# Optimization experiments

Measured on AMD Instinct MI355X. Metric: run time of the kernel, lower is better.

Reference implementation:

```python
import jax, jax.numpy as jnp
import numpy as np

B, C, H, W = 4, 256, 64, 64
CI = C // 2  # inter_channels


def setup_inputs() -> dict:
    key = jax.random.key(0)
    ks = jax.random.split(key, 10)
    s_in = 1.0 / np.sqrt(C)
    s_out = 1.0 / np.sqrt(CI)
    return {
        "rgbd": jax.random.normal(ks[0], (B, C, H, W), jnp.float32),
        "x": jax.random.normal(ks[1], (B, C, H, W), jnp.float32),
        "q_w": jax.random.uniform(ks[2], (CI, C), jnp.float32, -s_in, s_in),
        "q_b": jax.random.uniform(ks[3], (CI,), jnp.float32, -s_in, s_in),
        "k_w": jax.random.uniform(ks[4], (CI, C), jnp.float32, -s_in, s_in),
        "k_b": jax.random.uniform(ks[5], (CI,), jnp.float32, -s_in, s_in),
        "v_w": jax.random.uniform(ks[6], (CI, C), jnp.float32, -s_in, s_in),
        "v_b": jax.random.uniform(ks[7], (CI,), jnp.float32, -s_in, s_in),
        "out_w": jax.random.uniform(ks[8], (C, CI), jnp.float32, -s_out, s_out),
        "out_b": jax.random.uniform(ks[9], (C,), jnp.float32, -s_out, s_out),
    }


def reference(rgbd, x, q_w, q_b, k_w, k_b, v_w, v_b, out_w, out_b):
    b, c, h, w = rgbd.shape
    ci = q_w.shape[0]
    n = h * w
    # 1x1 convs == channel-wise linear maps; flatten spatial to tokens
    xs = x.reshape(b, c, n)        # [B, C, N]
    rs = rgbd.reshape(b, c, n)     # [B, C, N]
    q = jnp.einsum('oc,bcn->bno', q_w, xs) + q_b          # [B, N, CI]
    k = jnp.einsum('oc,bcn->bon', k_w, rs) + k_b[:, None]  # [B, CI, N]
    v = jnp.einsum('oc,bcn->bno', v_w, rs) + v_b          # [B, N, CI]
    attn = jax.nn.softmax(jnp.einsum('bqc,bck->bqk', q, k), axis=-1)  # [B, N, N]
    out = jnp.einsum('bqk,bkc->bqc', attn, v)             # [B, N, CI]
    out = jnp.einsum('oc,bnc->bon', out_w, out) + out_b[:, None]  # [B, C, N]
    return rgbd + out.reshape(b, c, h, w)
```

## Files before the change

### kernel.cpp

```cpp
#include <hip/hip_runtime.h>
#include <cstdint>
#include <cstddef>

typedef unsigned short u16;
typedef __attribute__((ext_vector_type(8))) short bf16x8;
typedef __attribute__((ext_vector_type(4))) float f32x4;
typedef __attribute__((ext_vector_type(16))) float f32x16;
typedef __attribute__((ext_vector_type(4))) uint32_t u32x4;

#define DEV __device__ __forceinline__

static constexpr float LOG2E = 1.4426950408889634f;

DEV u16 f2bf(float f) {
  uint32_t u = __float_as_uint(f);
  u += 0x7fffu + ((u >> 16) & 1u);
  return (u16)(u >> 16);
}
DEV float bf2f(u16 h) {
  uint32_t u = ((uint32_t)h) << 16;
  return __uint_as_float(u);
}
DEV uint32_t cvtpk(float lo, float hi) {
  uint32_t r;
  asm("v_cvt_pk_bf16_f32 %0, %1, %2" : "=v"(r) : "v"(lo), "v"(hi));
  return r;
}
DEV float exp2fast(float x) {
  float r;
  asm("v_exp_f32 %0, %1" : "=v"(r) : "v"(x));
  return r;
}
DEV void plswap(uint32_t& a, uint32_t& b) {
  asm("v_permlane32_swap_b32 %0, %1" : "+v"(a), "+v"(b));
}

DEV f32x4 mfma16(bf16x8 a, bf16x8 b, f32x4 c) {
  return __builtin_amdgcn_mfma_f32_16x16x32_bf16(a, b, c, 0, 0, 0);
}
DEV f32x16 mfma32(bf16x8 a, bf16x8 b, f32x16 c) {
  return __builtin_amdgcn_mfma_f32_32x32x16_bf16(a, b, c, 0, 0, 0);
}

DEV void gload_lds16(const void* g, void* l) {
  __builtin_amdgcn_global_load_lds(
      (const __attribute__((address_space(1))) uint32_t*)g,
      (__attribute__((address_space(3))) uint32_t*)l, 16, 0, 0);
}

static constexpr int BATCH = 4;
static constexpr int C = 256;
static constexpr int CI = 128;
static constexpr int N = 4096;
static constexpr int SPLIT = 4;

__global__ __launch_bounds__(256) void cvt_w(const float* __restrict__ a,
                                             const float* __restrict__ b,
                                             const float* __restrict__ c,
                                             const float* __restrict__ d,
                                             u16* __restrict__ oa, u16* __restrict__ ob,
                                             u16* __restrict__ oc, u16* __restrict__ od) {
  int i = blockIdx.x * 256 + threadIdx.x;
  oa[i] = f2bf(a[i] * LOG2E);
  ob[i] = f2bf(b[i]);
  oc[i] = f2bf(c[i]);
  od[i] = f2bf(d[i]);
}

__global__ __launch_bounds__(256) void proj_kernel(
    const float* __restrict__ x, const float* __restrict__ rgbd,
    const u16* __restrict__ Wq, const u16* __restrict__ Wk, const u16* __restrict__ Wv,
    const float* __restrict__ qb, const float* __restrict__ kb, const float* __restrict__ vb,
    u16* __restrict__ Qb, u16* __restrict__ Kb, u16* __restrict__ Vtb) {
  __shared__ __align__(16) u16 xT[64][C + 8];
  __shared__ __align__(16) u16 rT[64][C + 8];
  const int b = blockIdx.y;
  const int n0 = blockIdx.x * 64;
  const int t = threadIdx.x;
  {
    const int tok = t & 63, cp = (t >> 6) * 2;
    const float* xb = x + (size_t)b * C * N + n0;
    const float* rb = rgbd + (size_t)b * C * N + n0;
    for (int c0 = 0; c0 < C; c0 += 8) {
      int c = c0 + cp;
      *(uint32_t*)&xT[tok][c] = cvtpk(xb[(size_t)c * N + tok], xb[(size_t)(c + 1) * N + tok]);
      *(uint32_t*)&rT[tok][c] = cvtpk(rb[(size_t)c * N + tok], rb[(size_t)(c + 1) * N + tok]);
    }
  }
  __syncthreads();
  const int w = t >> 6, lane = t & 63, g = lane >> 4, cl = lane & 15;

#define PROJ_QK(Sarr, W, bias, Out, SCL)                                              \
  {                                                                                   \
    bf16x8 afr[8];                                                                    \
    _Pragma("unroll") for (int ks = 0; ks < 8; ++ks)                                  \
        afr[ks] = *(const bf16x8*)&Sarr[w * 16 + cl][ks * 32 + g * 8];                \
    _Pragma("unroll") for (int ct = 0; ct < 8; ++ct) {                                \
      f32x4 acc = {0.f, 0.f, 0.f, 0.f};                                               \
      _Pragma("unroll") for (int ks = 0; ks < 8; ++ks) {                              \
        bf16x8 bb = *(const bf16x8*)&W[(size_t)(ct * 16 + cl) * C + ks * 32 + g * 8]; \
        acc = mfma16(afr[ks], bb, acc);                                               \
      }                                                                               \
      float bv = bias[ct * 16 + cl] * (SCL);                                          \
      _Pragma("unroll") for (int r = 0; r < 4; ++r) {                                 \
        int tok = n0 + w * 16 + g * 4 + r;                                            \
        Out[((size_t)b * N + tok) * CI + ct * 16 + cl] = f2bf(acc[r] + bv);           \
      }                                                                               \
    }                                                                                 \
  }

  PROJ_QK(xT, Wq, qb, Qb, LOG2E)
  PROJ_QK(rT, Wk, kb, Kb, 1.0f)
#undef PROJ_QK

  #pragma unroll
  for (int rt = 0; rt < 2; ++rt) {
    bf16x8 aw[8];
    #pragma unroll
    for (int ks = 0; ks < 8; ++ks)
      aw[ks] = *(const bf16x8*)&Wv[(size_t)(w * 32 + rt * 16 + cl) * C + ks * 32 + g * 8];
    #pragma unroll
    for (int ct = 0; ct < 4; ++ct) {
      f32x4 acc = {0.f, 0.f, 0.f, 0.f};
      #pragma unroll
      for (int ks = 0; ks < 8; ++ks) {
        bf16x8 bb = *(const bf16x8*)&rT[ct * 16 + cl][ks * 32 + g * 8];
        acc = mfma16(aw[ks], bb, acc);
      }
      #pragma unroll
      for (int r = 0; r < 4; ++r) {
        int o = w * 32 + rt * 16 + g * 4 + r;
        Vtb[((size_t)b * CI + o) * N + n0 + ct * 16 + cl] = f2bf(acc[r] + vb[o]);
      }
    }
  }
}

template <int SPL>
__global__ __launch_bounds__(128, 2) void attn_kernel(
    const u16* __restrict__ Qb, const u16* __restrict__ Kb,
    const u16* __restrict__ Vtb, u16* __restrict__ Opart,
    float2* __restrict__ ml) {
  constexpr int KPB = N / SPL;
  constexpr int NT = KPB / 32;
  constexpr int CPX = 32 * SPL;
  __shared__ __align__(16) u16 Klds[2][32 * 128];
  __shared__ __align__(16) u16 Vlds[2][128 * 32];
  const int lin = blockIdx.x;
  const int nl = (lin & 7) * CPX + (lin >> 3);
  const int qi = nl & 63;
  const int grp = nl >> 6;
  const int b = grp & 3;
  const int s = grp >> 2;
  const int q0 = qi * 64;
  const int t = threadIdx.x;
  const int w = t >> 6, lane = t & 63;
  const int hi = lane >> 5, l31 = lane & 31;

  const u16* Kg = Kb + (size_t)b * N * CI;
  const u16* Vg = Vtb + (size_t)b * CI * N;

  const int v_ss = (t & 3) ^ ((t >> 3) & 3);
  const int wbase = (t & ~63);

#define STAGE_KV(bi, k0_)                                                         \
  do {                                                                            \
    _Pragma("unroll") for (int c = 0; c < 4; ++c) {                               \
      const int r = c * 8 + (t >> 4);                                             \
      const int ss = (t & 15) ^ (r & 15);                                         \
      gload_lds16(Kg + (size_t)((k0_) + r) * CI + ss * 8,                         \
                  &Klds[bi][(c * 128 + wbase) * 8]);                              \
    }                                                                             \
    _Pragma("unroll") for (int c = 0; c < 4; ++c) {                               \
      const int vr = c * 32 + (t >> 2);                                           \
      gload_lds16(Vg + (size_t)vr * N + (k0_) + v_ss * 8,                         \
                  &Vlds[bi][(c * 128 + wbase) * 8]);                              \
    }                                                                             \
  } while (0)

  const u16* Qg = Qb + ((size_t)b * N + q0 + w * 32 + l31) * CI;
  bf16x8 qf[8];
  #pragma unroll
  for (int mm = 0; mm < 8; ++mm)
    qf[mm] = *(const bf16x8*)(Qg + mm * 16 + hi * 8);
  asm volatile("s_waitcnt vmcnt(0)" ::: "memory");

  f32x16 oacc[4];
  #pragma unroll
  for (int ct = 0; ct < 4; ++ct)
    #pragma unroll
    for (int i = 0; i < 16; ++i) oacc[ct][i] = 0.f;
  float m_run = -1e30f, l_run = 0.f;

  const int kbeg = s * KPB;
  STAGE_KV(0, kbeg);
  STAGE_KV(1, kbeg + 32);

  int buf = 0;
  for (int tt = 0; tt < NT; ++tt) {
    asm volatile("s_waitcnt vmcnt(8)" ::: "memory");
    __builtin_amdgcn_s_barrier();
    const int knext = kbeg + ((tt + 2 < NT) ? tt + 2 : tt) * 32;

    bf16x8 kf[8];
    #pragma unroll
    for (int mm = 0; mm < 8; ++mm)
      kf[mm] = *(const bf16x8*)&Klds[buf][l31 * 128 + ((((mm << 1) | hi) ^ l31) & 15) * 8];
    bf16x8 vf[4][2];
    const int vsw = (l31 >> 1) & 3;
    #pragma unroll
    for (int ct = 0; ct < 4; ++ct)
      #pragma unroll
      for (int ks = 0; ks < 2; ++ks)
        vf[ct][ks] = *(const bf16x8*)
            &Vlds[buf][(32 * ct + l31) * 32 + ((((ks << 1) | hi) ^ vsw) & 3) * 8];
    asm volatile("s_waitcnt lgkmcnt(0)" ::: "memory");
    __builtin_amdgcn_sched_barrier(0);
    __builtin_amdgcn_s_barrier();
    STAGE_KV(buf, knext);

    f32x16 st;
    #pragma unroll
    for (int i = 0; i < 16; ++i) st[i] = 0.f;
    __builtin_amdgcn_s_setprio(1);
    #pragma unroll
    for (int mm = 0; mm < 8; ++mm) st = mfma32(kf[mm], qf[mm], st);
    __builtin_amdgcn_s_setprio(0);

    float tmax = st[0];
    #pragma unroll
    for (int i = 1; i < 16; ++i) tmax = fmaxf(tmax, st[i]);
    tmax = fmaxf(tmax, __shfl_xor(tmax, 32));
    if (!__all(tmax - m_run <= 11.5f)) {
      const float mn = fmaxf(m_run, tmax);
      const float alpha = exp2fast(m_run - mn);
      m_run = mn;
      l_run *= alpha;
      #pragma unroll
      for (int reg = 0; reg < 16; ++reg) {
        float ar = __shfl(alpha, (reg & 3) + 8 * (reg >> 2) + 4 * hi);
        oacc[0][reg] *= ar; oacc[1][reg] *= ar;
        oacc[2][reg] *= ar; oacc[3][reg] *= ar;
      }
    }
    float p[16];
    float ls = 0.f;
    #pragma unroll
    for (int i = 0; i < 16; ++i) {
      p[i] = exp2fast(st[i] - m_run);
      ls += p[i];
    }
    ls += __shfl_xor(ls, 32);
    l_run += ls;

    uint32_t d0 = cvtpk(p[0], p[1]),   e0 = cvtpk(p[4], p[5]);
    uint32_t d1 = cvtpk(p[2], p[3]),   e1 = cvtpk(p[6], p[7]);
    uint32_t d2 = cvtpk(p[8], p[9]),   e2 = cvtpk(p[12], p[13]);
    uint32_t d3 = cvtpk(p[10], p[11]), e3 = cvtpk(p[14], p[15]);
    plswap(d0, e0);
    plswap(d1, e1);
    plswap(d2, e2);
    plswap(d3, e3);
    u32x4 pw0 = {d0, d1, e0, e1};
    u32x4 pw1 = {d2, d3, e2, e3};
    bf16x8 pa0 = __builtin_bit_cast(bf16x8, pw0);
    bf16x8 pa1 = __builtin_bit_cast(bf16x8, pw1);

    __builtin_amdgcn_s_setprio(1);
    #pragma unroll
    for (int ct = 0; ct < 4; ++ct) {
      oacc[ct] = mfma32(pa0, vf[ct][0], oacc[ct]);
      oacc[ct] = mfma32(pa1, vf[ct][1], oacc[ct]);
    }
    __builtin_amdgcn_s_setprio(0);

    buf ^= 1;
  }
#undef STAGE_KV
  asm volatile("s_waitcnt vmcnt(0)" ::: "memory");

  const float inv = 1.0f / l_run;
  #pragma unroll
  for (int reg = 0; reg < 16; ++reg) {
    const int ql = (reg & 3) + 8 * (reg >> 2) + 4 * hi;
    const float invr = __shfl(inv, ql);
    const int q = q0 + w * 32 + ql;
    #pragma unroll
    for (int ct = 0; ct < 4; ++ct)
      Opart[(((size_t)(s * BATCH + b)) * N + q) * CI + 32 * ct + l31] =
          f2bf(oacc[ct][reg] * invr);
  }
  if (lane < 32) {
    const int q = q0 + w * 32 + lane;
    ml[(size_t)(s * BATCH + b) * N + q] = make_float2(m_run, l_run);
  }
}

__global__ __launch_bounds__(256) void outproj_kernel(
    const u16* __restrict__ Opart, const float2* __restrict__ ml,
    const u16* __restrict__ Wo, const float* __restrict__ obias,
    const float* __restrict__ rgbd, float* __restrict__ out) {
  __shared__ __align__(16) u16 ObL[64][CI + 8];
  const int b = blockIdx.y;
  const int n0 = blockIdx.x * 64;
  const int t = threadIdx.x;

  #pragma unroll
  for (int i = 0; i < 4; ++i) {
    const int idx = t + i * 256;
    const int row_l = idx >> 4, ci8 = idx & 15;
    const size_t row = (size_t)b * N + n0 + row_l;
    float2 sv[SPLIT];
    float M = -1e30f;
    #pragma unroll
    for (int sp = 0; sp < SPLIT; ++sp) {
      sv[sp] = ml[(size_t)sp * BATCH * N + row];
      M = fmaxf(M, sv[sp].x);
    }
    float wv[SPLIT], wsum = 0.f;
    #pragma unroll
    for (int sp = 0; sp < SPLIT; ++sp) {
      wv[sp] = sv[sp].y * exp2fast(sv[sp].x - M);
      wsum += wv[sp];
    }
    const float invL = 1.0f / wsum;
    float acc[8];
    #pragma unroll
    for (int j = 0; j < 8; ++j) acc[j] = 0.f;
    #pragma unroll
    for (int sp = 0; sp < SPLIT; ++sp) {
      const float wsc = wv[sp] * invL;
      bf16x8 v = *(const bf16x8*)&Opart[((size_t)sp * BATCH * N + row) * CI + ci8 * 8];
      #pragma unroll
      for (int j = 0; j < 8; ++j) acc[j] += wsc * bf2f((u16)v[j]);
    }
    bf16x8 o;
    #pragma unroll
    for (int j = 0; j < 8; ++j) o[j] = (short)f2bf(acc[j]);
    *(bf16x8*)&ObL[row_l][ci8 * 8] = o;
  }
  __syncthreads();

  const int w = t >> 6, lane = t & 63, g = lane >> 4, cl = lane & 15;
  f32x4 acc[4][4];
  #pragma unroll
  for (int i = 0; i < 4; ++i)
    #pragma unroll
    for (int j = 0; j < 4; ++j) acc[i][j] = {0.f, 0.f, 0.f, 0.f};

  #pragma unroll
  for (int ks = 0; ks < 4; ++ks) {
    bf16x8 bo[4];
    #pragma unroll
    for (int ct = 0; ct < 4; ++ct)
      bo[ct] = *(const bf16x8*)&ObL[ct * 16 + cl][ks * 32 + g * 8];
    #pragma unroll
    for (int rt = 0; rt < 4; ++rt) {
      bf16x8 aw = *(const bf16x8*)&Wo[(size_t)(w * 64 + rt * 16 + cl) * CI + ks * 32 + g * 8];
      #pragma unroll
      for (int ct = 0; ct < 4; ++ct) acc[rt][ct] = mfma16(aw, bo[ct], acc[rt][ct]);
    }
  }
  #pragma unroll
  for (int rt = 0; rt < 4; ++rt) {
    #pragma unroll
    for (int r = 0; r < 4; ++r) {
      const int o = w * 64 + rt * 16 + g * 4 + r;
      const float bb = obias[o];
      #pragma unroll
      for (int ct = 0; ct < 4; ++ct) {
        size_t idx = ((size_t)b * C + o) * N + n0 + ct * 16 + cl;
        out[idx] = rgbd[idx] + bb + acc[rt][ct][r];
      }
    }
  }
}

extern "C" void kernel_launch(void* const* d_in, const int* in_sizes, int n_in,
                              void* d_out, int out_size, void* d_ws, size_t ws_size,
                              hipStream_t stream) {
  (void)in_sizes; (void)n_in; (void)out_size; (void)ws_size;
  const float* rgbd = (const float*)d_in[0];
  const float* x    = (const float*)d_in[1];
  const float* q_w  = (const float*)d_in[2];
  const float* q_b  = (const float*)d_in[3];
  const float* k_w  = (const float*)d_in[4];
  const float* k_b  = (const float*)d_in[5];
  const float* v_w  = (const float*)d_in[6];
  const float* v_b  = (const float*)d_in[7];
  const float* o_w  = (const float*)d_in[8];
  const float* o_b  = (const float*)d_in[9];
  float* out = (float*)d_out;

  char* ws = (char*)d_ws;
  const size_t MB = 1024 * 1024;
  const size_t szQKV = (size_t)BATCH * N * CI * sizeof(u16);
  u16* Qb  = (u16*)(ws);
  u16* Kb  = (u16*)(ws + szQKV);
  u16* Vtb = (u16*)(ws + 2 * szQKV);
  u16* Wq  = (u16*)(ws + 3 * szQKV);
  u16* Wk  = Wq + (size_t)CI * C;
  u16* Wv  = Wk + (size_t)CI * C;
  u16* Wo  = Wv + (size_t)CI * C;
  u16* Opart = (u16*)(ws + 13 * MB);
  float2* ml = (float2*)(ws + 29 * MB);

  cvt_w<<<dim3((C * CI) / 256), 256, 0, stream>>>(q_w, k_w, v_w, o_w, Wq, Wk, Wv, Wo);
  proj_kernel<<<dim3(N / 64, BATCH), 256, 0, stream>>>(x, rgbd, Wq, Wk, Wv,
                                                       q_b, k_b, v_b, Qb, Kb, Vtb);
  attn_kernel<SPLIT><<<dim3(64 * BATCH * SPLIT), 128, 0, stream>>>(Qb, Kb, Vtb, Opart, ml);
  outproj_kernel<<<dim3(N / 64, BATCH), 256, 0, stream>>>(Opart, ml, Wo, o_b, rgbd, out);
}
```

Measured before the change: 93.81 us.

## Double attention block and KV tile sizes, interleave two softmax halves

The attention kernel now uses 256-thread blocks covering 128 queries and stages 64-key K/V tiles, so each staged tile is shared by four waves instead of two. It halves the grid and the number of barrier iterations. Each iteration splits into two 32-key halves, with the PV MFMAs of the first half overlapping the QK MFMAs of the second. The projection kernel is retiled to 32 tokens per block with an occupancy hint, giving more blocks. The cost is doubled LDS per attention block and higher register pressure, which may limit occupancy.

```diff
diff --git a/kernel.cpp b/kernel.cpp
--- a/kernel.cpp
+++ b/kernel.cpp
@@ -67,21 +67,22 @@
   od[i] = f2bf(d[i]);
 }
 
-__global__ __launch_bounds__(256) void proj_kernel(
+__global__ __launch_bounds__(256, 4) void proj_kernel(
     const float* __restrict__ x, const float* __restrict__ rgbd,
     const u16* __restrict__ Wq, const u16* __restrict__ Wk, const u16* __restrict__ Wv,
     const float* __restrict__ qb, const float* __restrict__ kb, const float* __restrict__ vb,
     u16* __restrict__ Qb, u16* __restrict__ Kb, u16* __restrict__ Vtb) {
-  __shared__ __align__(16) u16 xT[64][C + 8];
-  __shared__ __align__(16) u16 rT[64][C + 8];
+  __shared__ __align__(16) u16 xT[32][C + 8];
+  __shared__ __align__(16) u16 rT[32][C + 8];
   const int b = blockIdx.y;
-  const int n0 = blockIdx.x * 64;
+  const int n0 = blockIdx.x * 32;
   const int t = threadIdx.x;
   {
-    const int tok = t & 63, cp = (t >> 6) * 2;
+    const int tok = t & 31, cp = (t >> 5) * 2;
     const float* xb = x + (size_t)b * C * N + n0;
     const float* rb = rgbd + (size_t)b * C * N + n0;
-    for (int c0 = 0; c0 < C; c0 += 8) {
+    #pragma unroll
+    for (int c0 = 0; c0 < C; c0 += 16) {
       int c = c0 + cp;
       *(uint32_t*)&xT[tok][c] = cvtpk(xb[(size_t)c * N + tok], xb[(size_t)(c + 1) * N + tok]);
       *(uint32_t*)&rT[tok][c] = cvtpk(rb[(size_t)c * N + tok], rb[(size_t)(c + 1) * N + tok]);
@@ -89,22 +90,25 @@
   }
   __syncthreads();
   const int w = t >> 6, lane = t & 63, g = lane >> 4, cl = lane & 15;
+  const int tg = w & 1;
+  const int hf = w >> 1;
 
 #define PROJ_QK(Sarr, W, bias, Out, SCL)                                              \
   {                                                                                   \
     bf16x8 afr[8];                                                                    \
     _Pragma("unroll") for (int ks = 0; ks < 8; ++ks)                                  \
-        afr[ks] = *(const bf16x8*)&Sarr[w * 16 + cl][ks * 32 + g * 8];                \
-    _Pragma("unroll") for (int ct = 0; ct < 8; ++ct) {                                \
+        afr[ks] = *(const bf16x8*)&Sarr[tg * 16 + cl][ks * 32 + g * 8];               \
+    _Pragma("unroll") for (int ct = 0; ct < 4; ++ct) {                                \
+      const int ctt = hf * 4 + ct;                                                    \
       f32x4 acc = {0.f, 0.f, 0.f, 0.f};                                               \
       _Pragma("unroll") for (int ks = 0; ks < 8; ++ks) {                              \
-        bf16x8 bb = *(const bf16x8*)&W[(size_t)(ct * 16 + cl) * C + ks * 32 + g * 8]; \
-        acc = mfma16(afr[ks], bb, acc);                                               \
+        bf16x8 bb = *(const bf16x8*)&W[(size_t)(ctt * 16 + cl) * C + ks * 32 + g * 8];\
+      acc = mfma16(afr[ks], bb, acc);                                                 \
       }                                                                               \
-      float bv = bias[ct * 16 + cl] * (SCL);                                          \
+      float bv = bias[ctt * 16 + cl] * (SCL);                                         \
       _Pragma("unroll") for (int r = 0; r < 4; ++r) {                                 \
-        int tok = n0 + w * 16 + g * 4 + r;                                            \
-        Out[((size_t)b * N + tok) * CI + ct * 16 + cl] = f2bf(acc[r] + bv);           \
+        int tok = n0 + tg * 16 + g * 4 + r;                                           \
+        Out[((size_t)b * N + tok) * CI + ctt * 16 + cl] = f2bf(acc[r] + bv);          \
       }                                                                               \
     }                                                                                 \
   }
@@ -120,7 +124,7 @@
     for (int ks = 0; ks < 8; ++ks)
       aw[ks] = *(const bf16x8*)&Wv[(size_t)(w * 32 + rt * 16 + cl) * C + ks * 32 + g * 8];
     #pragma unroll
-    for (int ct = 0; ct < 4; ++ct) {
+    for (int ct = 0; ct < 2; ++ct) {
       f32x4 acc = {0.f, 0.f, 0.f, 0.f};
       #pragma unroll
       for (int ks = 0; ks < 8; ++ks) {
@@ -137,22 +141,22 @@
 }
 
 template <int SPL>
-__global__ __launch_bounds__(128, 2) void attn_kernel(
+__global__ __launch_bounds__(256, 2) void attn_kernel(
     const u16* __restrict__ Qb, const u16* __restrict__ Kb,
     const u16* __restrict__ Vtb, u16* __restrict__ Opart,
     float2* __restrict__ ml) {
   constexpr int KPB = N / SPL;
-  constexpr int NT = KPB / 32;
-  constexpr int CPX = 32 * SPL;
-  __shared__ __align__(16) u16 Klds[2][32 * 128];
-  __shared__ __align__(16) u16 Vlds[2][128 * 32];
+  constexpr int NT = KPB / 64;
+  constexpr int CPX = 16 * SPL;
+  __shared__ __align__(16) u16 Klds[2][64 * 128];
+  __shared__ __align__(16) u16 Vlds[2][128 * 64];
   const int lin = blockIdx.x;
   const int nl = (lin & 7) * CPX + (lin >> 3);
-  const int qi = nl & 63;
-  const int grp = nl >> 6;
+  const int qi = nl & 31;
+  const int grp = nl >> 5;
   const int b = grp & 3;
   const int s = grp >> 2;
-  const int q0 = qi * 64;
+  const int q0 = qi * 128;
   const int t = threadIdx.x;
   const int w = t >> 6, lane = t & 63;
   const int hi = lane >> 5, l31 = lane & 31;
@@ -160,21 +164,20 @@
   const u16* Kg = Kb + (size_t)b * N * CI;
   const u16* Vg = Vtb + (size_t)b * CI * N;
 
-  const int v_ss = (t & 3) ^ ((t >> 3) & 3);
-  const int wbase = (t & ~63);
+  const int k_ss = (t & 15) ^ ((t >> 4) & 15);
+  const int v_ss = (t & 7) ^ ((t >> 3) & 7);
 
 #define STAGE_KV(bi, k0_)                                                         \
   do {                                                                            \
     _Pragma("unroll") for (int c = 0; c < 4; ++c) {                               \
-      const int r = c * 8 + (t >> 4);                                             \
-      const int ss = (t & 15) ^ (r & 15);                                         \
-      gload_lds16(Kg + (size_t)((k0_) + r) * CI + ss * 8,                         \
-                  &Klds[bi][(c * 128 + wbase) * 8]);                              \
+      const int r = c * 16 + (t >> 4);                                            \
+      gload_lds16(Kg + (size_t)((k0_) + r) * CI + k_ss * 8,                       \
+                  &Klds[bi][(c * 256 + t) * 8]);                                  \
     }                                                                             \
     _Pragma("unroll") for (int c = 0; c < 4; ++c) {                               \
-      const int vr = c * 32 + (t >> 2);                                           \
+      const int vr = c * 32 + (t >> 3);                                           \
       gload_lds16(Vg + (size_t)vr * N + (k0_) + v_ss * 8,                         \
-                  &Vlds[bi][(c * 128 + wbase) * 8]);                              \
+                  &Vlds[bi][(c * 256 + t) * 8]);                                  \
     }                                                                             \
   } while (0)
 
@@ -194,89 +197,120 @@
 
   const int kbeg = s * KPB;
   STAGE_KV(0, kbeg);
-  STAGE_KV(1, kbeg + 32);
+  STAGE_KV(1, kbeg + 64);
+
+#define SOFTMAX_HALF(st, paX0, paX1)                                              \
+  {                                                                               \
+    float tmax = st[0];                                                           \
+    _Pragma("unroll") for (int i = 1; i < 16; ++i) tmax = fmaxf(tmax, st[i]);     \
+    tmax = fmaxf(tmax, __shfl_xor(tmax, 32));                                     \
+    if (!__all(tmax - m_run <= 11.5f)) {                                          \
+      const float mn = fmaxf(m_run, tmax);                                        \
+      const float alpha = exp2fast(m_run - mn);                                   \
+      m_run = mn;                                                                 \
+      l_run *= alpha;                                                             \
+      _Pragma("unroll") for (int reg = 0; reg < 16; ++reg) {                      \
+        float ar = __shfl(alpha, (reg & 3) + 8 * (reg >> 2) + 4 * hi);            \
+        oacc[0][reg] *= ar; oacc[1][reg] *= ar;                                   \
+        oacc[2][reg] *= ar; oacc[3][reg] *= ar;                                   \
+      }                                                                           \
+    }                                                                             \
+    float p[16], ls = 0.f;                                                        \
+    _Pragma("unroll") for (int i = 0; i < 16; ++i) {                              \
+      p[i] = exp2fast(st[i] - m_run);                                             \
+      ls += p[i];                                                                 \
+    }                                                                             \
+    ls += __shfl_xor(ls, 32);                                                     \
+    l_run += ls;                                                                  \
+    uint32_t d0 = cvtpk(p[0], p[1]),   e0 = cvtpk(p[4], p[5]);                    \
+    uint32_t d1 = cvtpk(p[2], p[3]),   e1 = cvtpk(p[6], p[7]);                    \
+    uint32_t d2 = cvtpk(p[8], p[9]),   e2 = cvtpk(p[12], p[13]);                  \
+    uint32_t d3 = cvtpk(p[10], p[11]), e3 = cvtpk(p[14], p[15]);                  \
+    plswap(d0, e0); plswap(d1, e1); plswap(d2, e2); plswap(d3, e3);               \
+    u32x4 pw0 = {d0, d1, e0, e1};                                                 \
+    u32x4 pw1 = {d2, d3, e2, e3};                                                 \
+    paX0 = __builtin_bit_cast(bf16x8, pw0);                                       \
+    paX1 = __builtin_bit_cast(bf16x8, pw1);                                       \
+  }
 
   int buf = 0;
   for (int tt = 0; tt < NT; ++tt) {
     asm volatile("s_waitcnt vmcnt(8)" ::: "memory");
     __builtin_amdgcn_s_barrier();
-    const int knext = kbeg + ((tt + 2 < NT) ? tt + 2 : tt) * 32;
-
-    bf16x8 kf[8];
+    const int knext = kbeg + ((tt + 2 < NT) ? tt + 2 : tt) * 64;
+
+    bf16x8 kfA[8];
     #pragma unroll
     for (int mm = 0; mm < 8; ++mm)
-      kf[mm] = *(const bf16x8*)&Klds[buf][l31 * 128 + ((((mm << 1) | hi) ^ l31) & 15) * 8];
-    bf16x8 vf[4][2];
-    const int vsw = (l31 >> 1) & 3;
+      kfA[mm] = *(const bf16x8*)&Klds[buf][l31 * 128 + ((((mm << 1) | hi) ^ (l31 & 15)) & 15) * 8];
+    asm volatile("s_waitcnt lgkmcnt(0)" ::: "memory");
+    __builtin_amdgcn_sched_barrier(0);
+
+    f32x16 st0;
+    #pragma unroll
+    for (int i = 0; i < 16; ++i) st0[i] = 0.f;
+    __builtin_amdgcn_s_setprio(1);
+    #pragma unroll
+    for (int mm = 0; mm < 8; ++mm) st0 = mfma32(kfA[mm], qf[mm], st0);
+    __builtin_amdgcn_s_setprio(0);
+
+    bf16x8 paA0, paA1;
+    SOFTMAX_HALF(st0, paA0, paA1)
+
+    bf16x8 kfB[8];
+    #pragma unroll
+    for (int mm = 0; mm < 8; ++mm)
+      kfB[mm] = *(const bf16x8*)&Klds[buf][(32 + l31) * 128 + ((((mm << 1) | hi) ^ (l31 & 15)) & 15) * 8];
+    bf16x8 vfA[4][2];
     #pragma unroll
     for (int ct = 0; ct < 4; ++ct)
       #pragma unroll
       for (int ks = 0; ks < 2; ++ks)
-        vf[ct][ks] = *(const bf16x8*)
-            &Vlds[buf][(32 * ct + l31) * 32 + ((((ks << 1) | hi) ^ vsw) & 3) * 8];
+        vfA[ct][ks] = *(const bf16x8*)
+            &Vlds[buf][(32 * ct + l31) * 64 + ((((ks << 1) | hi) ^ (l31 & 7)) & 7) * 8];
+    asm volatile("s_waitcnt lgkmcnt(0)" ::: "memory");
+    __builtin_amdgcn_sched_barrier(0);
+
+    f32x16 st1;
+    #pragma unroll
+    for (int i = 0; i < 16; ++i) st1[i] = 0.f;
+    __builtin_amdgcn_s_setprio(1);
+    #pragma unroll
+    for (int ct = 0; ct < 4; ++ct) {
+      oacc[ct] = mfma32(paA0, vfA[ct][0], oacc[ct]);
+      oacc[ct] = mfma32(paA1, vfA[ct][1], oacc[ct]);
+    }
+    #pragma unroll
+    for (int mm = 0; mm < 8; ++mm) st1 = mfma32(kfB[mm], qf[mm], st1);
+    __builtin_amdgcn_s_setprio(0);
+
+    bf16x8 paB0, paB1;
+    SOFTMAX_HALF(st1, paB0, paB1)
+
+    bf16x8 vfB[4][2];
+    #pragma unroll
+    for (int ct = 0; ct < 4; ++ct)
+      #pragma unroll
+      for (int ks = 0; ks < 2; ++ks)
+        vfB[ct][ks] = *(const bf16x8*)
+            &Vlds[buf][(32 * ct + l31) * 64 + (((4 + ((ks << 1) | hi)) ^ (l31 & 7)) & 7) * 8];
     asm volatile("s_waitcnt lgkmcnt(0)" ::: "memory");
     __builtin_amdgcn_sched_barrier(0);
     __builtin_amdgcn_s_barrier();
     STAGE_KV(buf, knext);
 
-    f32x16 st;
-    #pragma unroll
-    for (int i = 0; i < 16; ++i) st[i] = 0.f;
     __builtin_amdgcn_s_setprio(1);
     #pragma unroll
-    for (int mm = 0; mm < 8; ++mm) st = mfma32(kf[mm], qf[mm], st);
+    for (int ct = 0; ct < 4; ++ct) {
+      oacc[ct] = mfma32(paB0, vfB[ct][0], oacc[ct]);
+      oacc[ct] = mfma32(paB1, vfB[ct][1], oacc[ct]);
+    }
     __builtin_amdgcn_s_setprio(0);
 
-    float tmax = st[0];
-    #pragma unroll
-    for (int i = 1; i < 16; ++i) tmax = fmaxf(tmax, st[i]);
-    tmax = fmaxf(tmax, __shfl_xor(tmax, 32));
-    if (!__all(tmax - m_run <= 11.5f)) {
-      const float mn = fmaxf(m_run, tmax);
-      const float alpha = exp2fast(m_run - mn);
-      m_run = mn;
-      l_run *= alpha;
-      #pragma unroll
-      for (int reg = 0; reg < 16; ++reg) {
-        float ar = __shfl(alpha, (reg & 3) + 8 * (reg >> 2) + 4 * hi);
-        oacc[0][reg] *= ar; oacc[1][reg] *= ar;
-        oacc[2][reg] *= ar; oacc[3][reg] *= ar;
-      }
-    }
-    float p[16];
-    float ls = 0.f;
-    #pragma unroll
-    for (int i = 0; i < 16; ++i) {
-      p[i] = exp2fast(st[i] - m_run);
-      ls += p[i];
-    }
-    ls += __shfl_xor(ls, 32);
-    l_run += ls;
-
-    uint32_t d0 = cvtpk(p[0], p[1]),   e0 = cvtpk(p[4], p[5]);
-    uint32_t d1 = cvtpk(p[2], p[3]),   e1 = cvtpk(p[6], p[7]);
-    uint32_t d2 = cvtpk(p[8], p[9]),   e2 = cvtpk(p[12], p[13]);
-    uint32_t d3 = cvtpk(p[10], p[11]), e3 = cvtpk(p[14], p[15]);
-    plswap(d0, e0);
-    plswap(d1, e1);
-    plswap(d2, e2);
-    plswap(d3, e3);
-    u32x4 pw0 = {d0, d1, e0, e1};
-    u32x4 pw1 = {d2, d3, e2, e3};
-    bf16x8 pa0 = __builtin_bit_cast(bf16x8, pw0);
-    bf16x8 pa1 = __builtin_bit_cast(bf16x8, pw1);
-
-    __builtin_amdgcn_s_setprio(1);
-    #pragma unroll
-    for (int ct = 0; ct < 4; ++ct) {
-      oacc[ct] = mfma32(pa0, vf[ct][0], oacc[ct]);
-      oacc[ct] = mfma32(pa1, vf[ct][1], oacc[ct]);
-    }
-    __builtin_amdgcn_s_setprio(0);
-
     buf ^= 1;
   }
 #undef STAGE_KV
+#undef SOFTMAX_HALF
   asm volatile("s_waitcnt vmcnt(0)" ::: "memory");
 
   const float inv = 1.0f / l_run;
@@ -406,8 +440,8 @@
   float2* ml = (float2*)(ws + 29 * MB);
 
   cvt_w<<<dim3((C * CI) / 256), 256, 0, stream>>>(q_w, k_w, v_w, o_w, Wq, Wk, Wv, Wo);
-  proj_kernel<<<dim3(N / 64, BATCH), 256, 0, stream>>>(x, rgbd, Wq, Wk, Wv,
+  proj_kernel<<<dim3(N / 32, BATCH), 256, 0, stream>>>(x, rgbd, Wq, Wk, Wv,
                                                        q_b, k_b, v_b, Qb, Kb, Vtb);
-  attn_kernel<SPLIT><<<dim3(64 * BATCH * SPLIT), 128, 0, stream>>>(Qb, Kb, Vtb, Opart, ml);
+  attn_kernel<SPLIT><<<dim3(128 * SPLIT), 256, 0, stream>>>(Qb, Kb, Vtb, Opart, ml);
   outproj_kernel<<<dim3(N / 64, BATCH), 256, 0, stream>>>(Opart, ml, Wo, o_b, rgbd, out);
 }
```

Measured after the change: 94.58 us. About the same (+0.8%).
